# Performance work log

Measured on AMD Instinct MI355X. Metric: run time of the kernel, lower is better.

## Reference

```python
import jax, jax.numpy as jnp
import numpy as np

N_HEADS = 8
EPS = 1e-6


def setup_inputs() -> dict:
    key = jax.random.key(0)
    ks = jax.random.split(key, 9)
    B, L, E = 4, 4096, 512
    s = 1.0 / np.sqrt(E)
    return {
        "x": jax.random.normal(ks[0], (B, L, E), jnp.float32),
        "Wq": jax.random.normal(ks[1], (E, E), jnp.float32) * s,
        "bq": jax.random.normal(ks[2], (E,), jnp.float32) * 0.01,
        "Wk": jax.random.normal(ks[3], (E, E), jnp.float32) * s,
        "bk": jax.random.normal(ks[4], (E,), jnp.float32) * 0.01,
        "Wv": jax.random.normal(ks[5], (E, E), jnp.float32) * s,
        "bv": jax.random.normal(ks[6], (E,), jnp.float32) * 0.01,
        "Wo": jax.random.normal(ks[7], (E, E), jnp.float32) * s,
        "bo": jax.random.normal(ks[8], (E,), jnp.float32) * 0.01,
    }


def reference(x, Wq, bq, Wk, bk, Wv, bv, Wo, bo):
    # x: (B, L, E); self-attention so query = key = value = x
    B, L, E = x.shape
    H = N_HEADS
    d = E // H
    m = jnp.float32(L)  # m = max(src_len, tgt_len)

    # projections (torch Linear: x @ W.T + b), then ReLU feature map
    q = jax.nn.relu(x @ Wq.T + bq).reshape(B, L, H, d)
    k = jax.nn.relu(x @ Wk.T + bk).reshape(B, L, H, d)
    v = (x @ Wv.T + bv).reshape(B, L, H, d)

    # cosFormer positional reweighting: (pi/2) * i / m for i = 1..L
    idx = (jnp.pi / 2.0) * jnp.arange(1, L + 1, dtype=jnp.float32) / m  # (L,)
    sin = jnp.sin(idx)[None, :, None, None]  # (1, L, 1, 1)
    cos = jnp.cos(idx)[None, :, None, None]

    q_sin, q_cos = q * sin, q * cos
    k_sin, k_cos = k * sin, k * cos

    # non-causal linear attention: per-head kv state, O(L * d^2)
    kv_cos = jnp.einsum("blhk,blhd->bhkd", k_cos, v)  # (B, H, d, d)
    kv_sin = jnp.einsum("blhk,blhd->bhkd", k_sin, v)

    k_cos_sum = k_cos.sum(axis=1)  # (B, H, d)
    k_sin_sum = k_sin.sum(axis=1)

    z = 1.0 / jnp.maximum(
        jnp.einsum("blhd,bhd->blh", q_cos, k_cos_sum)
        + jnp.einsum("blhd,bhd->blh", q_sin, k_sin_sum),
        EPS,
    )  # (B, L, H)

    attn = (
        jnp.einsum("blhk,bhkd->blhd", q_cos, kv_cos)
        + jnp.einsum("blhk,bhkd->blhd", q_sin, kv_sin)
    ) * z[..., None]

    out = attn.reshape(B, L, E) @ Wo.T + bo  # (B, L, E)
    return out
```

## Files before the change

kernel.cpp:

```cpp
#include <hip/hip_runtime.h>
#include <hip/hip_bf16.h>

#define L_SEQ 4096
#define E_DIM 512
#define NHEAD 8
#define DHEAD 64
#define NBATCH 4
#define NROWS (NBATCH * L_SEQ)

typedef short bf16x8 __attribute__((ext_vector_type(8)));
typedef float f32x4 __attribute__((ext_vector_type(4)));

__device__ __forceinline__ float bf2f(ushort u) {
    union { float f; unsigned int i; } x;
    x.i = ((unsigned int)u) << 16;
    return x.f;
}
__device__ __forceinline__ ushort f2bf(float f) {
    unsigned int u = __float_as_uint(f);
    unsigned int r = 0x7fffu + ((u >> 16) & 1u);
    u += r;
    return (ushort)(u >> 16);
}

#define GLD16(gptr, lptr) \
    __builtin_amdgcn_global_load_lds( \
        (const __attribute__((address_space(1))) void*)(gptr), \
        (__attribute__((address_space(3))) void*)(lptr), 16, 0, 0)

#define BAR_LGKM() do { \
    asm volatile("s_waitcnt lgkmcnt(0)" ::: "memory"); \
    __builtin_amdgcn_sched_barrier(0); \
    __builtin_amdgcn_s_barrier(); \
    __builtin_amdgcn_sched_barrier(0); } while (0)

__global__ void convert_kernel(const float* __restrict__ in, ushort* __restrict__ out, int n4) {
    int stride = gridDim.x * blockDim.x;
    for (int i = blockIdx.x * blockDim.x + threadIdx.x; i < n4; i += stride) {
        float4 f = reinterpret_cast<const float4*>(in)[i];
        ushort4 o;
        o.x = f2bf(f.x); o.y = f2bf(f.y); o.z = f2bf(f.z); o.w = f2bf(f.w);
        reinterpret_cast<ushort4*>(out)[i] = o;
    }
}

__global__ __launch_bounds__(256) void convert_w_kernel(
    const float* __restrict__ w0, const float* __restrict__ w1,
    const float* __restrict__ w2, const float* __restrict__ w3,
    ushort* __restrict__ o0, ushort* __restrict__ o1,
    ushort* __restrict__ o2, ushort* __restrict__ o3,
    float* __restrict__ sintab, float* __restrict__ costab)
{
    const int tid = threadIdx.x;
    const int y = blockIdx.y;
    if (y == 4) {
        const int l = blockIdx.x * 256 + tid;
        if (blockIdx.x < 16) {
            const float ang = (float)(l + 1) * (1.5707963267948966f / (float)L_SEQ);
            sintab[l] = sinf(ang);
            costab[l] = cosf(ang);
        }
        return;
    }
    const float* in = (y == 0) ? w0 : (y == 1) ? w1 : (y == 2) ? w2 : w3;
    ushort* out = (y == 0) ? o0 : (y == 1) ? o1 : (y == 2) ? o2 : o3;
    const int i = blockIdx.x * 256 + tid;
    float4 f = reinterpret_cast<const float4*>(in)[i];
    ushort4 o;
    o.x = f2bf(f.x); o.y = f2bf(f.y); o.z = f2bf(f.z); o.w = f2bf(f.w);
    reinterpret_cast<ushort4*>(out)[i] = o;
}

__global__ __launch_bounds__(512) void gemm3_kernel(
    int modeBase, int nt,
    const ushort* __restrict__ xA, const ushort* __restrict__ oA,
    const ushort* __restrict__ wq, const ushort* __restrict__ wk,
    const ushort* __restrict__ wv, const ushort* __restrict__ wo,
    const float* __restrict__ bq, const float* __restrict__ bk,
    const float* __restrict__ bv, const float* __restrict__ bo,
    ushort* __restrict__ qb, ushort* __restrict__ kT, ushort* __restrict__ vT,
    float* __restrict__ outF)
{
    __shared__ ushort SH[66048];
    ushort* TS = SH + 49152;

    const int tid = threadIdx.x;
    const int lane = tid & 63;
    const int wid = tid >> 6;
    const int wm = wid >> 2;
    const int wn = wid & 3;
    const int p = blockIdx.x;
    const int rowBase = (p >> 1) * 128;
    const int colBase = (p & 1) * 256;

    const ushort* __restrict__ Ap = (modeBase == 3) ? oA : xA;

    const int fr = lane & 15;
    const int g = lane >> 4;
    const int fr7 = fr & 7;
    const int sc_row = tid >> 3;
    const int sc_ch  = tid & 7;
    const int totKt = nt * 8;

    f32x4 acc[4][4];
#pragma unroll
    for (int m = 0; m < 4; ++m)
#pragma unroll
        for (int n = 0; n < 4; ++n)
            acc[m][n] = (f32x4){0.f, 0.f, 0.f, 0.f};

    auto STAGE = [&](int gt2) {
        const int mode = modeBase + (gt2 >> 3);
        const ushort* __restrict__ W =
            (mode == 0) ? wq : (mode == 1) ? wk : (mode == 2) ? wv : wo;
        const int k0 = (gt2 & 7) * 64;
        const int bufb = (gt2 & 1) * 24576;
#pragma unroll
        for (int i = 0; i < 2; ++i) {
            const int row = i * 64 + sc_row;
            const int srcc = (sc_ch ^ (row & 7)) * 8;
            GLD16(&Ap[(size_t)(rowBase + row) * E_DIM + k0 + srcc],
                  &SH[bufb + (i * 512 + tid) * 8]);
        }
#pragma unroll
        for (int i = 0; i < 4; ++i) {
            const int row = i * 64 + sc_row;
            const int srcc = (sc_ch ^ (row & 7)) * 8;
            GLD16(&W[(size_t)(colBase + row) * E_DIM + k0 + srcc],
                  &SH[bufb + 8192 + (i * 512 + tid) * 8]);
        }
    };

    STAGE(0);
    STAGE(1);
    asm volatile("s_waitcnt vmcnt(6)" ::: "memory");
    __builtin_amdgcn_sched_barrier(0);
    __builtin_amdgcn_s_barrier();
    __builtin_amdgcn_sched_barrier(0);

    const int kch0 = (g ^ fr7) * 8;
    const int kch1 = ((4 + g) ^ fr7) * 8;
    const int aroff = (wm * 64 + fr) * 64;
    const int broff = 8192 + (wn * 64 + fr) * 64;
    const int b = rowBase >> 12;
    const int lloc = rowBase & (L_SEQ - 1);

    for (int gt = 0; gt < totKt; ++gt) {
        const int base = (gt & 1) * 24576;
        bf16x8 af[2][4], bfv[2][4];
#pragma unroll
        for (int m = 0; m < 4; ++m) {
            af[0][m] = *reinterpret_cast<const bf16x8*>(&SH[base + aroff + m * 1024 + kch0]);
            af[1][m] = *reinterpret_cast<const bf16x8*>(&SH[base + aroff + m * 1024 + kch1]);
        }
#pragma unroll
        for (int n = 0; n < 4; ++n) {
            bfv[0][n] = *reinterpret_cast<const bf16x8*>(&SH[base + broff + n * 1024 + kch0]);
            bfv[1][n] = *reinterpret_cast<const bf16x8*>(&SH[base + broff + n * 1024 + kch1]);
        }
        BAR_LGKM();

        if (gt + 2 < totKt) STAGE(gt + 2);

        __builtin_amdgcn_s_setprio(1);
#pragma unroll
        for (int kk = 0; kk < 2; ++kk)
#pragma unroll
            for (int m = 0; m < 4; ++m)
#pragma unroll
                for (int n = 0; n < 4; ++n)
                    acc[m][n] = __builtin_amdgcn_mfma_f32_16x16x32_bf16(
                        af[kk][m], bfv[kk][n], acc[m][n], 0, 0, 0);
        __builtin_amdgcn_s_setprio(0);
        __builtin_amdgcn_sched_barrier(0);

        if ((gt & 7) == 7) {
            const int mode = modeBase + (gt >> 3);
            const float* __restrict__ bias =
                (mode == 0) ? bq : (mode == 1) ? bk : (mode == 2) ? bv : bo;
            if (mode == 0) {
#pragma unroll
                for (int m = 0; m < 4; ++m)
#pragma unroll
                    for (int j = 0; j < 4; ++j) {
                        const int grow = rowBase + wm * 64 + m * 16 + g * 4 + j;
#pragma unroll
                        for (int n = 0; n < 4; ++n) {
                            const int gcol = colBase + wn * 64 + n * 16 + fr;
                            const float val = fmaxf(acc[m][n][j] + bias[gcol], 0.f);
                            qb[(size_t)grow * E_DIM + gcol] = f2bf(val);
                        }
                    }
            } else if (mode == 3) {
#pragma unroll
                for (int m = 0; m < 4; ++m)
#pragma unroll
                    for (int j = 0; j < 4; ++j) {
                        const int grow = rowBase + wm * 64 + m * 16 + g * 4 + j;
#pragma unroll
                        for (int n = 0; n < 4; ++n) {
                            const int gcol = colBase + wn * 64 + n * 16 + fr;
                            outF[(size_t)grow * E_DIM + gcol] = acc[m][n][j] + bias[gcol];
                        }
                    }
            } else {
                ushort* __restrict__ dstbuf = (mode == 1) ? kT : vT;
#pragma unroll
                for (int ph = 0; ph < 2; ++ph) {
                    BAR_LGKM();
                    if ((wn >> 1) == ph) {
#pragma unroll
                        for (int m = 0; m < 4; ++m)
#pragma unroll
                            for (int j = 0; j < 4; ++j) {
                                const int lr_ = wm * 64 + m * 16 + g * 4 + j;
#pragma unroll
                                for (int n = 0; n < 4; ++n) {
                                    const int fcl = (wn & 1) * 64 + n * 16 + fr;
                                    float val = acc[m][n][j] + bias[colBase + ph * 128 + fcl];
                                    if (mode == 1) val = fmaxf(val, 0.f);
                                    TS[fcl * 132 + lr_] = f2bf(val);
                                }
                            }
                    }
                    BAR_LGKM();
#pragma unroll
                    for (int i = 0; i < 4; ++i) {
                        const int c = i * 512 + tid;
                        const int r = c >> 4;
                        const int cc = c & 15;
                        const int gfeat = colBase + ph * 128 + r;
                        const size_t dst = ((size_t)(b * E_DIM + gfeat)) * L_SEQ + lloc + cc * 8;
                        *reinterpret_cast<uint4*>(&dstbuf[dst]) =
                            *reinterpret_cast<const uint4*>(&TS[r * 132 + cc * 8]);
                    }
                }
            }
#pragma unroll
            for (int m = 0; m < 4; ++m)
#pragma unroll
                for (int n = 0; n < 4; ++n)
                    acc[m][n] = (f32x4){0.f, 0.f, 0.f, 0.f};
        }

        if (gt < totKt - 1) {
            if (gt + 2 < totKt) asm volatile("s_waitcnt vmcnt(6)" ::: "memory");
            else                asm volatile("s_waitcnt vmcnt(0)" ::: "memory");
            __builtin_amdgcn_sched_barrier(0);
            __builtin_amdgcn_s_barrier();
            __builtin_amdgcn_sched_barrier(0);
        }
    }
}

__global__ __launch_bounds__(256) void kv_kernel(
    const ushort* __restrict__ kT, const ushort* __restrict__ vT,
    const float* __restrict__ sintab, const float* __restrict__ costab,
    float* __restrict__ kv_part, float* __restrict__ sum_part)
{
    const int chunk = blockIdx.x;
    const int bh = blockIdx.y;
    const int tid = threadIdx.x;
    const int lane = tid & 63;
    const int w = tid >> 6;
    const int fr = lane & 15;
    const int g = lane >> 4;

    const size_t tbase = (size_t)bh * 64 * L_SEQ;

    f32x4 acc[8], accS[8];
#pragma unroll
    for (int n = 0; n < 8; ++n) {
        acc[n] = (f32x4){0.f, 0.f, 0.f, 0.f};
        accS[n] = (f32x4){0.f, 0.f, 0.f, 0.f};
    }

    const int lchunk = chunk * (L_SEQ / 8);
    for (int l0 = lchunk; l0 < lchunk + (L_SEQ / 8); l0 += 32) {
        const int col = l0 + g * 8;
        bf16x8 vf = *reinterpret_cast<const bf16x8*>(&vT[tbase + (size_t)(w * 16 + fr) * L_SEQ + col]);
        bf16x8 kf[4];
#pragma unroll
        for (int n = 0; n < 4; ++n)
            kf[n] = *reinterpret_cast<const bf16x8*>(&kT[tbase + (size_t)(n * 16 + fr) * L_SEQ + col]);
        float4 c0 = *reinterpret_cast<const float4*>(&costab[col]);
        float4 c1 = *reinterpret_cast<const float4*>(&costab[col + 4]);
        float4 s0 = *reinterpret_cast<const float4*>(&sintab[col]);
        float4 s1 = *reinterpret_cast<const float4*>(&sintab[col + 4]);
        const float c8[8] = {c0.x, c0.y, c0.z, c0.w, c1.x, c1.y, c1.z, c1.w};
        const float s8[8] = {s0.x, s0.y, s0.z, s0.w, s1.x, s1.y, s1.z, s1.w};
        bf16x8 afc, afs, cw, sw;
#pragma unroll
        for (int e = 0; e < 8; ++e) {
            const float v = bf2f((ushort)vf[e]);
            afc[e] = (short)f2bf(v * c8[e]);
            afs[e] = (short)f2bf(v * s8[e]);
            cw[e]  = (short)f2bf(c8[e]);
            sw[e]  = (short)f2bf(s8[e]);
        }
#pragma unroll
        for (int n = 0; n < 4; ++n) {
            acc[n]      = __builtin_amdgcn_mfma_f32_16x16x32_bf16(afc, kf[n], acc[n], 0, 0, 0);
            acc[n + 4]  = __builtin_amdgcn_mfma_f32_16x16x32_bf16(afs, kf[n], acc[n + 4], 0, 0, 0);
            accS[n]     = __builtin_amdgcn_mfma_f32_16x16x32_bf16(cw,  kf[n], accS[n], 0, 0, 0);
            accS[n + 4] = __builtin_amdgcn_mfma_f32_16x16x32_bf16(sw,  kf[n], accS[n + 4], 0, 0, 0);
        }
    }

    const size_t pbase = ((size_t)(chunk * 32 + bh)) * 8192;
#pragma unroll
    for (int n = 0; n < 8; ++n)
#pragma unroll
        for (int j = 0; j < 4; ++j)
            kv_part[pbase + (size_t)(w * 16 + g * 4 + j) * 128 + n * 16 + fr] = acc[n][j];
    if (w == 0 && g == 0) {
        const size_t sbase = (size_t)(chunk * 32 + bh) * 128;
#pragma unroll
        for (int n = 0; n < 8; ++n)
            sum_part[sbase + n * 16 + fr] = accS[n][0];
    }
}

#define KVT_ROWS 80
#define KVT_STRIDE (KVT_ROWS * 128)
__global__ __launch_bounds__(256) void kv_reduce_kernel(
    const float* __restrict__ kv_part, const float* __restrict__ sum_part,
    ushort* __restrict__ kvT)
{
    const int bh = blockIdx.x;
    const int tid = threadIdx.x;
    ushort* kvb = kvT + (size_t)bh * KVT_STRIDE;
    for (int idx = tid; idx < 8192; idx += 256) {
        float s = 0.f;
#pragma unroll
        for (int c = 0; c < 8; ++c)
            s += kv_part[((size_t)(c * 32 + bh)) * 8192 + idx];
        kvb[idx] = f2bf(s);
    }
    if (tid < 128) {
        float s = 0.f;
#pragma unroll
        for (int c = 0; c < 8; ++c)
            s += sum_part[(size_t)(c * 32 + bh) * 128 + tid];
        const ushort hi = f2bf(s);
        const float lo = s - bf2f(hi);
        kvb[64 * 128 + tid] = hi;
        kvb[65 * 128 + tid] = f2bf(lo);
    }
    for (int idx = tid; idx < 14 * 128; idx += 256)
        kvb[66 * 128 + idx] = 0;
}

__global__ __launch_bounds__(256) void attn_kernel(
    const ushort* __restrict__ Qb, const ushort* __restrict__ kvT,
    const float* __restrict__ sintab, const float* __restrict__ costab,
    ushort* __restrict__ attn_out)
{
    const int bh = blockIdx.y;
    const int b = bh >> 3, h = bh & 7;
    const int tid = threadIdx.x;
    const int lane = tid & 63;
    const int w = tid >> 6;

    __shared__ ushort Bs[KVT_ROWS][136];

#pragma unroll
    for (int i = 0; i < 5; ++i) {
        const int c = i * 256 + tid;
        const int d = c >> 4, cc = c & 15;
        *reinterpret_cast<uint4*>(&Bs[d][cc * 8]) =
            *reinterpret_cast<const uint4*>(&kvT[(size_t)bh * KVT_STRIDE + (size_t)c * 8]);
    }
    __syncthreads();

    const int rowBase = blockIdx.x * 256 + w * 64;
    const int fr = lane & 15;
    const int g = lane >> 4;

    float cvm[4], svm[4];
#pragma unroll
    for (int m = 0; m < 4; ++m) {
        const int l = (rowBase + m * 16 + fr) & (L_SEQ - 1);
        cvm[m] = costab[l];
        svm[m] = sintab[l];
    }

    f32x4 acc[4][5];
#pragma unroll
    for (int m = 0; m < 4; ++m)
#pragma unroll
        for (int n = 0; n < 5; ++n)
            acc[m][n] = (f32x4){0.f, 0.f, 0.f, 0.f};

#pragma unroll
    for (int ks = 0; ks < 4; ++ks) {
        const int kk = (ks & 1) * 32 + g * 8;
        const int kcomb = ks * 32 + g * 8;

        bf16x8 af[4];
#pragma unroll
        for (int m = 0; m < 4; ++m) {
            const int r = rowBase + m * 16 + fr;
            bf16x8 qf = *reinterpret_cast<const bf16x8*>(
                &Qb[((size_t)(b * L_SEQ) + r) * E_DIM + h * DHEAD + kk]);
            const float sc = (ks < 2) ? cvm[m] : svm[m];
#pragma unroll
            for (int e = 0; e < 8; ++e)
                af[m][e] = (short)f2bf(bf2f((ushort)qf[e]) * sc);
        }

        bf16x8 bfr[5];
#pragma unroll
        for (int n = 0; n < 5; ++n)
            bfr[n] = *reinterpret_cast<const bf16x8*>(&Bs[n * 16 + fr][kcomb]);
#pragma unroll
        for (int m = 0; m < 4; ++m)
#pragma unroll
            for (int n = 0; n < 5; ++n)
                acc[m][n] = __builtin_amdgcn_mfma_f32_16x16x32_bf16(af[m], bfr[n], acc[m][n], 0, 0, 0);
    }

#pragma unroll
    for (int m = 0; m < 4; ++m) {
#pragma unroll
        for (int j = 0; j < 4; ++j) {
            const float den = __shfl(acc[m][4][j], g * 16 + 0) + __shfl(acc[m][4][j], g * 16 + 1);
            const float z = 1.f / fmaxf(den, 1e-6f);
            const int grow = rowBase + m * 16 + g * 4 + j;
            const size_t obase = ((size_t)(b * L_SEQ) + grow) * E_DIM + h * DHEAD;
#pragma unroll
            for (int n = 0; n < 4; ++n)
                attn_out[obase + n * 16 + fr] = f2bf(acc[m][n][j] * z);
        }
    }
}

extern "C" void kernel_launch(void* const* d_in, const int* in_sizes, int n_in,
                              void* d_out, int out_size, void* d_ws, size_t ws_size,
                              hipStream_t stream) {
    const float* x  = (const float*)d_in[0];
    const float* Wq = (const float*)d_in[1];
    const float* bq = (const float*)d_in[2];
    const float* Wk = (const float*)d_in[3];
    const float* bk = (const float*)d_in[4];
    const float* Wv = (const float*)d_in[5];
    const float* bv = (const float*)d_in[6];
    const float* Wo = (const float*)d_in[7];
    const float* bo = (const float*)d_in[8];
    float* out = (float*)d_out;

    char* ws = (char*)d_ws;
    size_t off = 0;
    auto alloc = [&](size_t bytes) -> char* {
        char* p = ws + off;
        off += (bytes + 255) & ~(size_t)255;
        return p;
    };

    const size_t big = (size_t)NROWS * E_DIM * sizeof(ushort);
    ushort* xb  = (ushort*)alloc(big);
    ushort* wqb = (ushort*)alloc(512 * 512 * sizeof(ushort));
    ushort* wkb = (ushort*)alloc(512 * 512 * sizeof(ushort));
    ushort* wvb = (ushort*)alloc(512 * 512 * sizeof(ushort));
    ushort* wob = (ushort*)alloc(512 * 512 * sizeof(ushort));
    ushort* qb  = (ushort*)alloc(big);
    ushort* kT  = (ushort*)alloc(big);
    ushort* vT  = (ushort*)alloc(big);
    float* kv_part  = (float*)alloc((size_t)8 * 32 * 8192 * sizeof(float));
    float* sum_part = (float*)alloc((size_t)8 * 32 * 128 * sizeof(float));
    ushort* kvT     = (ushort*)alloc((size_t)32 * KVT_STRIDE * sizeof(ushort));
    float* sintab   = (float*)alloc(L_SEQ * sizeof(float));
    float* costab   = (float*)alloc(L_SEQ * sizeof(float));
    ushort* attnb = kT;

    convert_kernel<<<2048, 256, 0, stream>>>(x, xb, NROWS * E_DIM / 4);
    convert_w_kernel<<<dim3(256, 5), 256, 0, stream>>>(
        Wq, Wk, Wv, Wo, wqb, wkb, wvb, wob, sintab, costab);

    gemm3_kernel<<<256, 512, 0, stream>>>(
        0, 3, xb, nullptr, wqb, wkb, wvb, wob, bq, bk, bv, bo,
        qb, kT, vT, nullptr);

    kv_kernel<<<dim3(8, 32), 256, 0, stream>>>(kT, vT, sintab, costab, kv_part, sum_part);
    kv_reduce_kernel<<<32, 256, 0, stream>>>(kv_part, sum_part, kvT);

    attn_kernel<<<dim3(16, 32), 256, 0, stream>>>(qb, kvT, sintab, costab, attnb);

    gemm3_kernel<<<256, 512, 0, stream>>>(
        3, 1, xb, attnb, wqb, wkb, wvb, wob, bq, bk, bv, bo,
        nullptr, nullptr, nullptr, out);
}
```

Before: 111.0 us.

## Fuse x bf16 conversion into QKV GEMM and use direct-load GEMM kernels

Removes the separate pass that converts x to bf16 and instead converts the fp32 x fragments in registers inside a new QKV projection kernel. Both projection GEMMs are replaced with simpler kernels that read operands straight from global memory into MFMA fragments, dropping the LDS double-buffered staging. The grid also changes to 128x128 tiles over a 128x4 grid of 256-thread blocks. This saves a full read and write of x and one launch, at the cost of uncoalesced, unstaged global loads: x is read as fp32 once per column block, and the staged-pipeline overlap is lost.

```diff
diff --git a/kernel.cpp b/kernel.cpp
--- a/kernel.cpp
+++ b/kernel.cpp
@@ -21,27 +21,6 @@
     unsigned int r = 0x7fffu + ((u >> 16) & 1u);
     u += r;
     return (ushort)(u >> 16);
-}
-
-#define GLD16(gptr, lptr) \
-    __builtin_amdgcn_global_load_lds( \
-        (const __attribute__((address_space(1))) void*)(gptr), \
-        (__attribute__((address_space(3))) void*)(lptr), 16, 0, 0)
-
-#define BAR_LGKM() do { \
-    asm volatile("s_waitcnt lgkmcnt(0)" ::: "memory"); \
-    __builtin_amdgcn_sched_barrier(0); \
-    __builtin_amdgcn_s_barrier(); \
-    __builtin_amdgcn_sched_barrier(0); } while (0)
-
-__global__ void convert_kernel(const float* __restrict__ in, ushort* __restrict__ out, int n4) {
-    int stride = gridDim.x * blockDim.x;
-    for (int i = blockIdx.x * blockDim.x + threadIdx.x; i < n4; i += stride) {
-        float4 f = reinterpret_cast<const float4*>(in)[i];
-        ushort4 o;
-        o.x = f2bf(f.x); o.y = f2bf(f.y); o.z = f2bf(f.z); o.w = f2bf(f.w);
-        reinterpret_cast<ushort4*>(out)[i] = o;
-    }
 }
 
 __global__ __launch_bounds__(256) void convert_w_kernel(
@@ -71,36 +50,138 @@
     reinterpret_cast<ushort4*>(out)[i] = o;
 }
 
-__global__ __launch_bounds__(512) void gemm3_kernel(
-    int modeBase, int nt,
-    const ushort* __restrict__ xA, const ushort* __restrict__ oA,
-    const ushort* __restrict__ wq, const ushort* __restrict__ wk,
-    const ushort* __restrict__ wv, const ushort* __restrict__ wo,
-    const float* __restrict__ bq, const float* __restrict__ bk,
-    const float* __restrict__ bv, const float* __restrict__ bo,
-    ushort* __restrict__ qb, ushort* __restrict__ kT, ushort* __restrict__ vT,
-    float* __restrict__ outF)
-{
-    __shared__ ushort SH[66048];
-    ushort* TS = SH + 49152;
+__global__ __launch_bounds__(256) void qkv2_kernel(
+    const float* __restrict__ x,
+    const ushort* __restrict__ wq, const ushort* __restrict__ wk, const ushort* __restrict__ wv,
+    const float* __restrict__ bq, const float* __restrict__ bk, const float* __restrict__ bv,
+    ushort* __restrict__ qb, ushort* __restrict__ kT, ushort* __restrict__ vT)
+{
+    __shared__ ushort TS[128 * 136];
 
     const int tid = threadIdx.x;
     const int lane = tid & 63;
     const int wid = tid >> 6;
-    const int wm = wid >> 2;
-    const int wn = wid & 3;
-    const int p = blockIdx.x;
-    const int rowBase = (p >> 1) * 128;
-    const int colBase = (p & 1) * 256;
-
-    const ushort* __restrict__ Ap = (modeBase == 3) ? oA : xA;
-
+    const int wm = wid >> 1, wn = wid & 1;
+    const int rowBase = blockIdx.x * 128;
+    const int colBase = blockIdx.y * 128;
     const int fr = lane & 15;
     const int g = lane >> 4;
-    const int fr7 = fr & 7;
-    const int sc_row = tid >> 3;
-    const int sc_ch  = tid & 7;
-    const int totKt = nt * 8;
+
+    const ushort* Wsel[3] = {wq, wk, wv};
+    const float* Bsel[3] = {bq, bk, bv};
+
+    const float* xrow[4];
+#pragma unroll
+    for (int m = 0; m < 4; ++m)
+        xrow[m] = &x[(size_t)(rowBase + wm * 64 + m * 16 + fr) * E_DIM + g * 8];
+    const ushort* wrow_off[4];
+
+    const int b = rowBase >> 12;
+    const int lloc = rowBase & (L_SEQ - 1);
+
+    for (int mode = 0; mode < 3; ++mode) {
+        const ushort* __restrict__ W = Wsel[mode];
+        const float* __restrict__ bias = Bsel[mode];
+#pragma unroll
+        for (int n = 0; n < 4; ++n)
+            wrow_off[n] = &W[(size_t)(colBase + wn * 64 + n * 16 + fr) * E_DIM + g * 8];
+
+        f32x4 acc[4][4];
+#pragma unroll
+        for (int m = 0; m < 4; ++m)
+#pragma unroll
+            for (int n = 0; n < 4; ++n)
+                acc[m][n] = (f32x4){0.f, 0.f, 0.f, 0.f};
+
+#pragma unroll
+        for (int ks = 0; ks < 16; ++ks) {
+            const int k0 = ks * 32;
+            bf16x8 af[4], bfr[4];
+#pragma unroll
+            for (int m = 0; m < 4; ++m) {
+                f32x4 lo = *reinterpret_cast<const f32x4*>(xrow[m] + k0);
+                f32x4 hi = *reinterpret_cast<const f32x4*>(xrow[m] + k0 + 4);
+#pragma unroll
+                for (int e = 0; e < 4; ++e) {
+                    af[m][e]     = (short)f2bf(lo[e]);
+                    af[m][e + 4] = (short)f2bf(hi[e]);
+                }
+            }
+#pragma unroll
+            for (int n = 0; n < 4; ++n)
+                bfr[n] = *reinterpret_cast<const bf16x8*>(wrow_off[n] + k0);
+#pragma unroll
+            for (int m = 0; m < 4; ++m)
+#pragma unroll
+                for (int n = 0; n < 4; ++n)
+                    acc[m][n] = __builtin_amdgcn_mfma_f32_16x16x32_bf16(
+                        af[m], bfr[n], acc[m][n], 0, 0, 0);
+        }
+
+        if (mode == 0) {
+#pragma unroll
+            for (int m = 0; m < 4; ++m)
+#pragma unroll
+                for (int j = 0; j < 4; ++j) {
+                    const int grow = rowBase + wm * 64 + m * 16 + g * 4 + j;
+#pragma unroll
+                    for (int n = 0; n < 4; ++n) {
+                        const int gcol = colBase + wn * 64 + n * 16 + fr;
+                        const float val = fmaxf(acc[m][n][j] + bias[gcol], 0.f);
+                        qb[(size_t)grow * E_DIM + gcol] = f2bf(val);
+                    }
+                }
+        } else {
+            ushort* __restrict__ dstbuf = (mode == 1) ? kT : vT;
+#pragma unroll
+            for (int m = 0; m < 4; ++m)
+#pragma unroll
+                for (int j = 0; j < 4; ++j) {
+                    const int lr_ = wm * 64 + m * 16 + g * 4 + j;
+#pragma unroll
+                    for (int n = 0; n < 4; ++n) {
+                        const int fcl = wn * 64 + n * 16 + fr;
+                        float val = acc[m][n][j] + bias[colBase + fcl];
+                        if (mode == 1) val = fmaxf(val, 0.f);
+                        TS[fcl * 136 + lr_] = f2bf(val);
+                    }
+                }
+            __syncthreads();
+#pragma unroll
+            for (int i = 0; i < 8; ++i) {
+                const int c = i * 256 + tid;
+                const int r = c >> 4;
+                const int cc = c & 15;
+                const size_t dst = ((size_t)(b * E_DIM + colBase + r)) * L_SEQ + lloc + cc * 8;
+                *reinterpret_cast<uint4*>(&dstbuf[dst]) =
+                    *reinterpret_cast<const uint4*>(&TS[r * 136 + cc * 8]);
+            }
+            __syncthreads();
+        }
+    }
+}
+
+__global__ __launch_bounds__(256) void out2_kernel(
+    const ushort* __restrict__ A, const ushort* __restrict__ W,
+    const float* __restrict__ bias, float* __restrict__ outF)
+{
+    const int tid = threadIdx.x;
+    const int lane = tid & 63;
+    const int wid = tid >> 6;
+    const int wm = wid >> 1, wn = wid & 1;
+    const int rowBase = blockIdx.x * 128;
+    const int colBase = blockIdx.y * 128;
+    const int fr = lane & 15;
+    const int g = lane >> 4;
+
+    const ushort* arow[4];
+    const ushort* wrow[4];
+#pragma unroll
+    for (int m = 0; m < 4; ++m)
+        arow[m] = &A[(size_t)(rowBase + wm * 64 + m * 16 + fr) * E_DIM + g * 8];
+#pragma unroll
+    for (int n = 0; n < 4; ++n)
+        wrow[n] = &W[(size_t)(colBase + wn * 64 + n * 16 + fr) * E_DIM + g * 8];
 
     f32x4 acc[4][4];
 #pragma unroll
@@ -109,148 +190,35 @@
         for (int n = 0; n < 4; ++n)
             acc[m][n] = (f32x4){0.f, 0.f, 0.f, 0.f};
 
-    auto STAGE = [&](int gt2) {
-        const int mode = modeBase + (gt2 >> 3);
-        const ushort* __restrict__ W =
-            (mode == 0) ? wq : (mode == 1) ? wk : (mode == 2) ? wv : wo;
-        const int k0 = (gt2 & 7) * 64;
-        const int bufb = (gt2 & 1) * 24576;
-#pragma unroll
-        for (int i = 0; i < 2; ++i) {
-            const int row = i * 64 + sc_row;
-            const int srcc = (sc_ch ^ (row & 7)) * 8;
-            GLD16(&Ap[(size_t)(rowBase + row) * E_DIM + k0 + srcc],
-                  &SH[bufb + (i * 512 + tid) * 8]);
-        }
-#pragma unroll
-        for (int i = 0; i < 4; ++i) {
-            const int row = i * 64 + sc_row;
-            const int srcc = (sc_ch ^ (row & 7)) * 8;
-            GLD16(&W[(size_t)(colBase + row) * E_DIM + k0 + srcc],
-                  &SH[bufb + 8192 + (i * 512 + tid) * 8]);
-        }
-    };
-
-    STAGE(0);
-    STAGE(1);
-    asm volatile("s_waitcnt vmcnt(6)" ::: "memory");
-    __builtin_amdgcn_sched_barrier(0);
-    __builtin_amdgcn_s_barrier();
-    __builtin_amdgcn_sched_barrier(0);
-
-    const int kch0 = (g ^ fr7) * 8;
-    const int kch1 = ((4 + g) ^ fr7) * 8;
-    const int aroff = (wm * 64 + fr) * 64;
-    const int broff = 8192 + (wn * 64 + fr) * 64;
-    const int b = rowBase >> 12;
-    const int lloc = rowBase & (L_SEQ - 1);
-
-    for (int gt = 0; gt < totKt; ++gt) {
-        const int base = (gt & 1) * 24576;
-        bf16x8 af[2][4], bfv[2][4];
-#pragma unroll
-        for (int m = 0; m < 4; ++m) {
-            af[0][m] = *reinterpret_cast<const bf16x8*>(&SH[base + aroff + m * 1024 + kch0]);
-            af[1][m] = *reinterpret_cast<const bf16x8*>(&SH[base + aroff + m * 1024 + kch1]);
-        }
-#pragma unroll
-        for (int n = 0; n < 4; ++n) {
-            bfv[0][n] = *reinterpret_cast<const bf16x8*>(&SH[base + broff + n * 1024 + kch0]);
-            bfv[1][n] = *reinterpret_cast<const bf16x8*>(&SH[base + broff + n * 1024 + kch1]);
-        }
-        BAR_LGKM();
-
-        if (gt + 2 < totKt) STAGE(gt + 2);
-
-        __builtin_amdgcn_s_setprio(1);
-#pragma unroll
-        for (int kk = 0; kk < 2; ++kk)
-#pragma unroll
-            for (int m = 0; m < 4; ++m)
-#pragma unroll
-                for (int n = 0; n < 4; ++n)
-                    acc[m][n] = __builtin_amdgcn_mfma_f32_16x16x32_bf16(
-                        af[kk][m], bfv[kk][n], acc[m][n], 0, 0, 0);
-        __builtin_amdgcn_s_setprio(0);
-        __builtin_amdgcn_sched_barrier(0);
-
-        if ((gt & 7) == 7) {
-            const int mode = modeBase + (gt >> 3);
-            const float* __restrict__ bias =
-                (mode == 0) ? bq : (mode == 1) ? bk : (mode == 2) ? bv : bo;
-            if (mode == 0) {
-#pragma unroll
-                for (int m = 0; m < 4; ++m)
-#pragma unroll
-                    for (int j = 0; j < 4; ++j) {
-                        const int grow = rowBase + wm * 64 + m * 16 + g * 4 + j;
-#pragma unroll
-                        for (int n = 0; n < 4; ++n) {
-                            const int gcol = colBase + wn * 64 + n * 16 + fr;
-                            const float val = fmaxf(acc[m][n][j] + bias[gcol], 0.f);
-                            qb[(size_t)grow * E_DIM + gcol] = f2bf(val);
-                        }
-                    }
-            } else if (mode == 3) {
-#pragma unroll
-                for (int m = 0; m < 4; ++m)
-#pragma unroll
-                    for (int j = 0; j < 4; ++j) {
-                        const int grow = rowBase + wm * 64 + m * 16 + g * 4 + j;
-#pragma unroll
-                        for (int n = 0; n < 4; ++n) {
-                            const int gcol = colBase + wn * 64 + n * 16 + fr;
-                            outF[(size_t)grow * E_DIM + gcol] = acc[m][n][j] + bias[gcol];
-                        }
-                    }
-            } else {
-                ushort* __restrict__ dstbuf = (mode == 1) ? kT : vT;
-#pragma unroll
-                for (int ph = 0; ph < 2; ++ph) {
-                    BAR_LGKM();
-                    if ((wn >> 1) == ph) {
-#pragma unroll
-                        for (int m = 0; m < 4; ++m)
-#pragma unroll
-                            for (int j = 0; j < 4; ++j) {
-                                const int lr_ = wm * 64 + m * 16 + g * 4 + j;
-#pragma unroll
-                                for (int n = 0; n < 4; ++n) {
-                                    const int fcl = (wn & 1) * 64 + n * 16 + fr;
-                                    float val = acc[m][n][j] + bias[colBase + ph * 128 + fcl];
-                                    if (mode == 1) val = fmaxf(val, 0.f);
-                                    TS[fcl * 132 + lr_] = f2bf(val);
-                                }
-                            }
-                    }
-                    BAR_LGKM();
-#pragma unroll
-                    for (int i = 0; i < 4; ++i) {
-                        const int c = i * 512 + tid;
-                        const int r = c >> 4;
-                        const int cc = c & 15;
-                        const int gfeat = colBase + ph * 128 + r;
-                        const size_t dst = ((size_t)(b * E_DIM + gfeat)) * L_SEQ + lloc + cc * 8;
-                        *reinterpret_cast<uint4*>(&dstbuf[dst]) =
-                            *reinterpret_cast<const uint4*>(&TS[r * 132 + cc * 8]);
-                    }
-                }
+#pragma unroll
+    for (int ks = 0; ks < 16; ++ks) {
+        const int k0 = ks * 32;
+        bf16x8 af[4], bfr[4];
+#pragma unroll
+        for (int m = 0; m < 4; ++m)
+            af[m] = *reinterpret_cast<const bf16x8*>(arow[m] + k0);
+#pragma unroll
+        for (int n = 0; n < 4; ++n)
+            bfr[n] = *reinterpret_cast<const bf16x8*>(wrow[n] + k0);
+#pragma unroll
+        for (int m = 0; m < 4; ++m)
+#pragma unroll
+            for (int n = 0; n < 4; ++n)
+                acc[m][n] = __builtin_amdgcn_mfma_f32_16x16x32_bf16(
+                    af[m], bfr[n], acc[m][n], 0, 0, 0);
+    }
+
+#pragma unroll
+    for (int m = 0; m < 4; ++m)
+#pragma unroll
+        for (int j = 0; j < 4; ++j) {
+            const int grow = rowBase + wm * 64 + m * 16 + g * 4 + j;
+#pragma unroll
+            for (int n = 0; n < 4; ++n) {
+                const int gcol = colBase + wn * 64 + n * 16 + fr;
+                outF[(size_t)grow * E_DIM + gcol] = acc[m][n][j] + bias[gcol];
             }
-#pragma unroll
-            for (int m = 0; m < 4; ++m)
-#pragma unroll
-                for (int n = 0; n < 4; ++n)
-                    acc[m][n] = (f32x4){0.f, 0.f, 0.f, 0.f};
-        }
-
-        if (gt < totKt - 1) {
-            if (gt + 2 < totKt) asm volatile("s_waitcnt vmcnt(6)" ::: "memory");
-            else                asm volatile("s_waitcnt vmcnt(0)" ::: "memory");
-            __builtin_amdgcn_sched_barrier(0);
-            __builtin_amdgcn_s_barrier();
-            __builtin_amdgcn_sched_barrier(0);
-        }
-    }
+        }
 }
 
 __global__ __launch_bounds__(256) void kv_kernel(
@@ -458,7 +426,6 @@
     };
 
     const size_t big = (size_t)NROWS * E_DIM * sizeof(ushort);
-    ushort* xb  = (ushort*)alloc(big);
     ushort* wqb = (ushort*)alloc(512 * 512 * sizeof(ushort));
     ushort* wkb = (ushort*)alloc(512 * 512 * sizeof(ushort));
     ushort* wvb = (ushort*)alloc(512 * 512 * sizeof(ushort));
@@ -473,20 +440,16 @@
     float* costab   = (float*)alloc(L_SEQ * sizeof(float));
     ushort* attnb = kT;
 
-    convert_kernel<<<2048, 256, 0, stream>>>(x, xb, NROWS * E_DIM / 4);
     convert_w_kernel<<<dim3(256, 5), 256, 0, stream>>>(
         Wq, Wk, Wv, Wo, wqb, wkb, wvb, wob, sintab, costab);
 
-    gemm3_kernel<<<256, 512, 0, stream>>>(
-        0, 3, xb, nullptr, wqb, wkb, wvb, wob, bq, bk, bv, bo,
-        qb, kT, vT, nullptr);
+    qkv2_kernel<<<dim3(128, 4), 256, 0, stream>>>(
+        x, wqb, wkb, wvb, bq, bk, bv, qb, kT, vT);
 
     kv_kernel<<<dim3(8, 32), 256, 0, stream>>>(kT, vT, sintab, costab, kv_part, sum_part);
     kv_reduce_kernel<<<32, 256, 0, stream>>>(kv_part, sum_part, kvT);
 
     attn_kernel<<<dim3(16, 32), 256, 0, stream>>>(qb, kvT, sintab, costab, attnb);
 
-    gemm3_kernel<<<256, 512, 0, stream>>>(
-        3, 1, xb, attnb, wqb, wkb, wvb, wob, bq, bk, bv, bo,
-        nullptr, nullptr, nullptr, out);
-}
+    out2_kernel<<<dim3(128, 4), 256, 0, stream>>>(attnb, wob, bo, out);
+}
```

Result: slower. 192.2 us (+73.1%).

## Rework projection GEMM into triple-buffered K=32 pipeline with templated modes

Applied to the files above, without the earlier changes.

The fused projection GEMM now uses K-tiles of 32 instead of 64, with three LDS buffers instead of two and a new XOR swizzle for 32-wide rows. The prefetch for tile gt+2 is issued before the LDS reads of the current tile, which removes the extra barrier between reads and staging. Mode and tile count become template parameters so the selects are resolved at compile time. LDS use drops, which may allow more overlap, but there are twice as many barriers and MFMA groups per tile are smaller.

```diff
diff --git a/kernel.cpp b/kernel.cpp
--- a/kernel.cpp
+++ b/kernel.cpp
@@ -71,9 +71,9 @@
     reinterpret_cast<ushort4*>(out)[i] = o;
 }
 
-__global__ __launch_bounds__(512) void gemm3_kernel(
-    int modeBase, int nt,
-    const ushort* __restrict__ xA, const ushort* __restrict__ oA,
+template<int MODE_BASE, int NT>
+__global__ __launch_bounds__(512) void gemm4_kernel(
+    const ushort* __restrict__ A,
     const ushort* __restrict__ wq, const ushort* __restrict__ wk,
     const ushort* __restrict__ wv, const ushort* __restrict__ wo,
     const float* __restrict__ bq, const float* __restrict__ bk,
@@ -81,8 +81,8 @@
     ushort* __restrict__ qb, ushort* __restrict__ kT, ushort* __restrict__ vT,
     float* __restrict__ outF)
 {
-    __shared__ ushort SH[66048];
-    ushort* TS = SH + 49152;
+    __shared__ ushort SH[36864 + 16896];
+    ushort* TS = SH + 36864;
 
     const int tid = threadIdx.x;
     const int lane = tid & 63;
@@ -92,15 +92,26 @@
     const int p = blockIdx.x;
     const int rowBase = (p >> 1) * 128;
     const int colBase = (p & 1) * 256;
-
-    const ushort* __restrict__ Ap = (modeBase == 3) ? oA : xA;
-
     const int fr = lane & 15;
     const int g = lane >> 4;
-    const int fr7 = fr & 7;
-    const int sc_row = tid >> 3;
-    const int sc_ch  = tid & 7;
-    const int totKt = nt * 8;
+    constexpr int TOT = NT * 16;
+
+    const int a_row = tid >> 2, a_s = tid & 3;
+    const int a_src = (a_s ^ (a_row & 3) ^ ((a_row >> 2) & 3)) * 8;
+    const int b_row0 = tid >> 2, b_s0 = tid & 3;
+    const int b_src0 = (b_s0 ^ (b_row0 & 3) ^ ((b_row0 >> 2) & 3)) * 8;
+    const int b_row1 = (512 + tid) >> 2, b_s1 = tid & 3;
+    const int b_src1 = (b_s1 ^ (b_row1 & 3) ^ ((b_row1 >> 2) & 3)) * 8;
+
+    auto STAGE = [&](int gt2, int bufb) {
+        const int mode = MODE_BASE + (gt2 >> 4);
+        const ushort* __restrict__ W =
+            (mode == 0) ? wq : (mode == 1) ? wk : (mode == 2) ? wv : wo;
+        const int k0 = (gt2 & 15) * 32;
+        GLD16(&A[(size_t)(rowBase + a_row) * E_DIM + k0 + a_src], &SH[bufb + tid * 8]);
+        GLD16(&W[(size_t)(colBase + b_row0) * E_DIM + k0 + b_src0], &SH[bufb + 4096 + tid * 8]);
+        GLD16(&W[(size_t)(colBase + b_row1) * E_DIM + k0 + b_src1], &SH[bufb + 4096 + (512 + tid) * 8]);
+    };
 
     f32x4 acc[4][4];
 #pragma unroll
@@ -109,73 +120,49 @@
         for (int n = 0; n < 4; ++n)
             acc[m][n] = (f32x4){0.f, 0.f, 0.f, 0.f};
 
-    auto STAGE = [&](int gt2) {
-        const int mode = modeBase + (gt2 >> 3);
-        const ushort* __restrict__ W =
-            (mode == 0) ? wq : (mode == 1) ? wk : (mode == 2) ? wv : wo;
-        const int k0 = (gt2 & 7) * 64;
-        const int bufb = (gt2 & 1) * 24576;
-#pragma unroll
-        for (int i = 0; i < 2; ++i) {
-            const int row = i * 64 + sc_row;
-            const int srcc = (sc_ch ^ (row & 7)) * 8;
-            GLD16(&Ap[(size_t)(rowBase + row) * E_DIM + k0 + srcc],
-                  &SH[bufb + (i * 512 + tid) * 8]);
-        }
-#pragma unroll
-        for (int i = 0; i < 4; ++i) {
-            const int row = i * 64 + sc_row;
-            const int srcc = (sc_ch ^ (row & 7)) * 8;
-            GLD16(&W[(size_t)(colBase + row) * E_DIM + k0 + srcc],
-                  &SH[bufb + 8192 + (i * 512 + tid) * 8]);
-        }
-    };
-
-    STAGE(0);
-    STAGE(1);
-    asm volatile("s_waitcnt vmcnt(6)" ::: "memory");
+    STAGE(0, 0);
+    STAGE(1, 12288);
+    asm volatile("s_waitcnt vmcnt(3)" ::: "memory");
     __builtin_amdgcn_sched_barrier(0);
     __builtin_amdgcn_s_barrier();
     __builtin_amdgcn_sched_barrier(0);
 
-    const int kch0 = (g ^ fr7) * 8;
-    const int kch1 = ((4 + g) ^ fr7) * 8;
-    const int aroff = (wm * 64 + fr) * 64;
-    const int broff = 8192 + (wn * 64 + fr) * 64;
+    const int sRead = (g ^ (fr & 3) ^ ((fr >> 2) & 3)) * 8;
+    const int aroff = (wm * 64 + fr) * 32 + sRead;
+    const int broff = 4096 + (wn * 64 + fr) * 32 + sRead;
     const int b = rowBase >> 12;
     const int lloc = rowBase & (L_SEQ - 1);
 
-    for (int gt = 0; gt < totKt; ++gt) {
-        const int base = (gt & 1) * 24576;
-        bf16x8 af[2][4], bfv[2][4];
-#pragma unroll
-        for (int m = 0; m < 4; ++m) {
-            af[0][m] = *reinterpret_cast<const bf16x8*>(&SH[base + aroff + m * 1024 + kch0]);
-            af[1][m] = *reinterpret_cast<const bf16x8*>(&SH[base + aroff + m * 1024 + kch1]);
-        }
-#pragma unroll
-        for (int n = 0; n < 4; ++n) {
-            bfv[0][n] = *reinterpret_cast<const bf16x8*>(&SH[base + broff + n * 1024 + kch0]);
-            bfv[1][n] = *reinterpret_cast<const bf16x8*>(&SH[base + broff + n * 1024 + kch1]);
-        }
-        BAR_LGKM();
-
-        if (gt + 2 < totKt) STAGE(gt + 2);
+    int cur = 0;
+    for (int gt = 0; gt < TOT; ++gt) {
+        const int bufb = cur * 12288;
+        if (gt + 2 < TOT) {
+            const int st = (cur == 0) ? 2 : cur - 1;
+            STAGE(gt + 2, st * 12288);
+        }
+        bf16x8 af[4], bfv[4];
+#pragma unroll
+        for (int m = 0; m < 4; ++m)
+            af[m] = *reinterpret_cast<const bf16x8*>(&SH[bufb + aroff + m * 512]);
+#pragma unroll
+        for (int n = 0; n < 4; ++n)
+            bfv[n] = *reinterpret_cast<const bf16x8*>(&SH[bufb + broff + n * 512]);
+        asm volatile("s_waitcnt lgkmcnt(0)" ::: "memory");
+        __builtin_amdgcn_sched_barrier(0);
 
         __builtin_amdgcn_s_setprio(1);
 #pragma unroll
-        for (int kk = 0; kk < 2; ++kk)
-#pragma unroll
-            for (int m = 0; m < 4; ++m)
-#pragma unroll
-                for (int n = 0; n < 4; ++n)
-                    acc[m][n] = __builtin_amdgcn_mfma_f32_16x16x32_bf16(
-                        af[kk][m], bfv[kk][n], acc[m][n], 0, 0, 0);
+        for (int m = 0; m < 4; ++m)
+#pragma unroll
+            for (int n = 0; n < 4; ++n)
+                acc[m][n] = __builtin_amdgcn_mfma_f32_16x16x32_bf16(
+                    af[m], bfv[n], acc[m][n], 0, 0, 0);
         __builtin_amdgcn_s_setprio(0);
         __builtin_amdgcn_sched_barrier(0);
 
-        if ((gt & 7) == 7) {
-            const int mode = modeBase + (gt >> 3);
+        const bool epi = ((gt & 15) == 15);
+        if (epi) {
+            const int mode = MODE_BASE + (gt >> 4);
             const float* __restrict__ bias =
                 (mode == 0) ? bq : (mode == 1) ? bk : (mode == 2) ? bv : bo;
             if (mode == 0) {
@@ -243,13 +230,14 @@
                     acc[m][n] = (f32x4){0.f, 0.f, 0.f, 0.f};
         }
 
-        if (gt < totKt - 1) {
-            if (gt + 2 < totKt) asm volatile("s_waitcnt vmcnt(6)" ::: "memory");
-            else                asm volatile("s_waitcnt vmcnt(0)" ::: "memory");
+        if (gt < TOT - 1) {
+            if (epi || gt + 2 >= TOT) asm volatile("s_waitcnt vmcnt(0)" ::: "memory");
+            else                      asm volatile("s_waitcnt vmcnt(3)" ::: "memory");
             __builtin_amdgcn_sched_barrier(0);
             __builtin_amdgcn_s_barrier();
             __builtin_amdgcn_sched_barrier(0);
         }
+        cur = (cur == 2) ? 0 : cur + 1;
     }
 }
 
@@ -477,16 +465,14 @@
     convert_w_kernel<<<dim3(256, 5), 256, 0, stream>>>(
         Wq, Wk, Wv, Wo, wqb, wkb, wvb, wob, sintab, costab);
 
-    gemm3_kernel<<<256, 512, 0, stream>>>(
-        0, 3, xb, nullptr, wqb, wkb, wvb, wob, bq, bk, bv, bo,
-        qb, kT, vT, nullptr);
+    gemm4_kernel<0, 3><<<256, 512, 0, stream>>>(
+        xb, wqb, wkb, wvb, wob, bq, bk, bv, bo, qb, kT, vT, nullptr);
 
     kv_kernel<<<dim3(8, 32), 256, 0, stream>>>(kT, vT, sintab, costab, kv_part, sum_part);
     kv_reduce_kernel<<<32, 256, 0, stream>>>(kv_part, sum_part, kvT);
 
     attn_kernel<<<dim3(16, 32), 256, 0, stream>>>(qb, kvT, sintab, costab, attnb);
 
-    gemm3_kernel<<<256, 512, 0, stream>>>(
-        3, 1, xb, attnb, wqb, wkb, wvb, wob, bq, bk, bv, bo,
-        nullptr, nullptr, nullptr, out);
-}
+    gemm4_kernel<3, 1><<<256, 512, 0, stream>>>(
+        attnb, wqb, wkb, wvb, wob, bq, bk, bv, bo, nullptr, nullptr, nullptr, out);
+}
```

Measured after the change: 112.5 us. No clear change (+1.4%).
